# Optimization experiments

Hardware: AMD Instinct MI355X
Metric: run time of the kernel (lower is better)

Reference implementation:

```python
import jax, jax.numpy as jnp
import numpy as np

TAU_MIN, TAU_MAX = 1.5, 4.0
NUM_EXPERTS, TOP_K = 8, 2
V_TH = 1.0
BN_EPS = 1e-5
SG_ALPHA = 4.0  # spikingjelly Sigmoid surrogate default

@jax.custom_vjp
def spike(v):
    # Heaviside spike with sigmoid surrogate gradient
    return (v >= 0.0).astype(v.dtype)

def _spike_fwd(v):
    return spike(v), v

def _spike_bwd(v, g):
    s = jax.nn.sigmoid(SG_ALPHA * v)
    return (g * SG_ALPHA * s * (1.0 - s),)

spike.defvjp(_spike_fwd, _spike_bwd)

def lif(x, tau):
    # MultiStepLIFNode, v_reset=0 (hard reset), detach_reset=True. x: (T, ...)
    def step(v, xt):
        v = v + (xt - v) / tau          # charge
        s = spike(v - V_TH)             # fire
        v = v * (1.0 - jax.lax.stop_gradient(s))  # detached hard reset
        return v, s
    return jax.lax.scan(step, jnp.zeros_like(x[0]), x)[1]

def conv1x1(x, W, b):
    # x: (T,B,Cin,H,W), W: (Cout,Cin) -> (T,B,Cout,H,W)
    return jnp.einsum('tbchw,oc->tbohw', x, W) + b[None, None, :, None, None]

def bn_eval(x, scale, bias):
    # eval-mode BatchNorm2d with running_mean=0, running_var=1
    inv = scale / jnp.sqrt(1.0 + BN_EPS)
    return x * inv[None, None, :, None, None] + bias[None, None, :, None, None]

def expert_fwd(x, tau, W1, b1, s1, bb1, W2, b2, s2, bb2):
    # MS_MLP_Expert: LIF -> conv1x1 -> BN -> (+res) -> LIF -> conv1x1 -> BN -> (+res)
    identity = x
    h = lif(x, tau)
    h = bn_eval(conv1x1(h, W1, b1), s1, bb1)
    h = identity + h            # res: in_features == hidden_features
    identity = h
    o = lif(h, tau)
    o = bn_eval(conv1x1(o, W2, b2), s2, bb2)
    return o + identity

def moe_forward(x, router_W, router_b, router_bn_scale, router_bn_bias,
                W1, b1, bn1_scale, bn1_bias, W2, b2, bn2_scale, bn2_bias):
    T, B, C, H, W = x.shape
    taus = jnp.linspace(TAU_MIN, TAU_MAX, NUM_EXPERTS).astype(x.dtype)
    # --- SpikeRouter ---
    r = lif(x, 2.0)
    r = bn_eval(conv1x1(r, router_W, router_b), router_bn_scale, router_bn_bias)  # (T,B,E,H,W)
    logits_tb = r.mean(axis=(-2, -1))          # (T,B,E)
    # batch-level temporal routing: aggregate logits over T
    logits = logits_tb.mean(axis=0)            # (B,E)
    probs = jax.nn.softmax(logits, axis=-1)
    topw, topi = jax.lax.top_k(probs, TOP_K)   # (B,k)
    topw = topw / topw.sum(axis=-1, keepdims=True)
    dense_w = jnp.zeros((B, NUM_EXPERTS), dtype=x.dtype).at[
        jnp.arange(B)[:, None], topi].set(topw)  # (B,E)
    # --- experts: each processes the full temporal sequence ---
    ys = jax.vmap(expert_fwd, in_axes=(None, 0, 0, 0, 0, 0, 0, 0, 0, 0))(
        x, taus, W1, b1, bn1_scale, bn1_bias, W2, b2, bn2_scale, bn2_bias)  # (E,T,B,C,H,W)
    out = jnp.einsum('etbchw,be->tbchw', ys, dense_w)
    return out

def setup_inputs() -> dict:
    key = jax.random.key(0)
    ks = jax.random.split(key, 6)
    T, B, C, H, Wd = 4, 16, 384, 16, 16
    E = NUM_EXPERTS
    wscale = 1.0 / np.sqrt(C)
    return {
        'x': jax.random.normal(ks[0], (T, B, C, H, Wd), jnp.float32),
        'router_W': jax.random.normal(ks[1], (E, C), jnp.float32) * wscale,
        'router_b': jnp.zeros((E,), jnp.float32),
        'router_bn_scale': jnp.ones((E,), jnp.float32),
        'router_bn_bias': jnp.zeros((E,), jnp.float32),
        'W1': jax.random.normal(ks[2], (E, C, C), jnp.float32) * wscale,
        'b1': jnp.zeros((E, C), jnp.float32),
        'bn1_scale': jnp.ones((E, C), jnp.float32),
        'bn1_bias': jnp.zeros((E, C), jnp.float32),
        'W2': jax.random.normal(ks[3], (E, C, C), jnp.float32) * wscale,
        'b2': jnp.zeros((E, C), jnp.float32),
        'bn2_scale': jnp.ones((E, C), jnp.float32),
        'bn2_bias': jnp.zeros((E, C), jnp.float32),
    }

def reference(x, router_W, router_b, router_bn_scale, router_bn_bias,
              W1, b1, bn1_scale, bn1_bias, W2, b2, bn2_scale, bn2_bias):
    return moe_forward(x, router_W, router_b, router_bn_scale, router_bn_bias,
                       W1, b1, bn1_scale, bn1_bias, W2, b2, bn2_scale, bn2_bias)
```

## Files before the change

### kernel.cpp

```cpp
#include <hip/hip_runtime.h>
#include <math.h>

#define T_  4
#define B_  16
#define C_  384
#define HW_ 256
#define E_  8

typedef __attribute__((ext_vector_type(8))) __bf16 bf16x8;
typedef __attribute__((ext_vector_type(4))) float f32x4;

union FragU { uint4 u; bf16x8 v; };

__device__ __forceinline__ float tau_of(int e) {
    if (e == 7) return 4.0f;
    const float delta = 2.5f / 7.0f;
    return __fadd_rn(1.5f, __fmul_rn((float)e, delta));
}

__device__ __forceinline__ FragU expand_mask(unsigned m) {
    FragU f;
    f.u.x = ((m & 1u)   ? 0x3F80u : 0u) | ((m & 2u)   ? 0x3F800000u : 0u);
    f.u.y = ((m & 4u)   ? 0x3F80u : 0u) | ((m & 8u)   ? 0x3F800000u : 0u);
    f.u.z = ((m & 16u)  ? 0x3F80u : 0u) | ((m & 32u)  ? 0x3F800000u : 0u);
    f.u.w = ((m & 64u)  ? 0x3F80u : 0u) | ((m & 128u) ? 0x3F800000u : 0u);
    return f;
}

__global__ __launch_bounds__(256) void k_prep(const float* __restrict__ x,
        const float* __restrict__ W1, const float* __restrict__ W2,
        unsigned short* __restrict__ Whif, unsigned short* __restrict__ Wlof,
        float* __restrict__ m) {
    if (blockIdx.x < 1152) {
        int tid = blockIdx.x * 256 + threadIdx.x;
        int l = tid & 63;
        int f = tid >> 6;
        int osub = f % 24;
        int ksub = (f / 24) % 12;
        int cv = (f / 288) & 1;
        int e = f / 576;
        const float* Wsrc = (cv == 0 ? W1 : W2) + (size_t)e * C_ * C_;
        int o = osub * 16 + (l & 15);
        int c0 = ksub * 32 + (l >> 4) * 8;
        const float* src = Wsrc + (size_t)o * C_ + c0;
        unsigned hw[8], lw[8];
#pragma unroll
        for (int j = 0; j < 8; ++j) {
            float w = src[j];
            unsigned u = __float_as_uint(w);
            unsigned hi = (u + 0x7FFFu + ((u >> 16) & 1u)) >> 16;
            float hf = __uint_as_float(hi << 16);
            float res = __fsub_rn(w, hf);
            unsigned ru = __float_as_uint(res);
            unsigned lo = (ru + 0x7FFFu + ((ru >> 16) & 1u)) >> 16;
            hw[j] = hi & 0xFFFFu;
            lw[j] = lo & 0xFFFFu;
        }
        size_t dst = (size_t)f * 512 + (size_t)l * 8;
        uint4 hv = make_uint4(hw[0] | (hw[1] << 16), hw[2] | (hw[3] << 16),
                              hw[4] | (hw[5] << 16), hw[6] | (hw[7] << 16));
        uint4 lv = make_uint4(lw[0] | (lw[1] << 16), lw[2] | (lw[3] << 16),
                              lw[4] | (lw[5] << 16), lw[6] | (lw[7] << 16));
        *reinterpret_cast<uint4*>(Whif + dst) = hv;
        *reinterpret_cast<uint4*>(Wlof + dst) = lv;
    } else {
        int bc = blockIdx.x - 1152;
        int b = bc / C_, c = bc % C_;
        int p = threadIdx.x;
        int wv = threadIdx.x >> 6;
        __shared__ int cnt[T_][4];
        float v = 0.0f;
#pragma unroll
        for (int t = 0; t < T_; ++t) {
            float xv = x[((t * B_ + b) * C_ + c) * HW_ + p];
            v = __fadd_rn(v, __fdiv_rn(__fsub_rn(xv, v), 2.0f));
            bool s = (__fsub_rn(v, 1.0f) >= 0.0f);
            if (s) v = 0.0f;
            unsigned long long mask = __ballot(s);
            if ((threadIdx.x & 63) == 0) cnt[t][wv] = (int)__popcll(mask);
        }
        __syncthreads();
        if (threadIdx.x < T_) {
            int t = threadIdx.x;
            int tot = cnt[t][0] + cnt[t][1] + cnt[t][2] + cnt[t][3];
            m[(t * B_ + b) * C_ + c] = (float)tot * 0.00390625f;
        }
    }
}

__device__ __forceinline__ void conv_mfma2(const unsigned short* __restrict__ Whif,
                                           const unsigned short* __restrict__ Wlof,
                                           unsigned base,
                                           const unsigned char* __restrict__ sf,
                                           f32x4 (&acc)[3][4],
                                           int wv, int lane) {
    const unsigned lane8 = (unsigned)lane * 8u;
    const unsigned wbase = base + (unsigned)(wv * 3) * 512u + lane8;
    const unsigned char* fp = sf + lane * 16;
    FragU c0f, c1f, c2f, n0f, n1f, n2f, bf[T_];
    c0f.u = *reinterpret_cast<const uint4*>(Wlof + wbase);
    c1f.u = *reinterpret_cast<const uint4*>(Wlof + wbase + 512u);
    c2f.u = *reinterpret_cast<const uint4*>(Wlof + wbase + 1024u);
#pragma unroll 1
    for (int ksub = 0; ksub < 12; ++ksub) {
        unsigned fo = wbase + (unsigned)ksub * 24u * 512u;
        const unsigned char* fk = fp + ksub * 4096;
#pragma unroll
        for (int t = 0; t < T_; ++t)
            bf[t].u = *reinterpret_cast<const uint4*>(fk + t * 1024);
        n0f.u = *reinterpret_cast<const uint4*>(Whif + fo);
        n1f.u = *reinterpret_cast<const uint4*>(Whif + fo + 512u);
        n2f.u = *reinterpret_cast<const uint4*>(Whif + fo + 1024u);
#pragma unroll
        for (int t = 0; t < T_; ++t) {
            acc[0][t] = __builtin_amdgcn_mfma_f32_16x16x32_bf16(c0f.v, bf[t].v, acc[0][t], 0, 0, 0);
            acc[1][t] = __builtin_amdgcn_mfma_f32_16x16x32_bf16(c1f.v, bf[t].v, acc[1][t], 0, 0, 0);
            acc[2][t] = __builtin_amdgcn_mfma_f32_16x16x32_bf16(c2f.v, bf[t].v, acc[2][t], 0, 0, 0);
        }
        if (ksub < 11) {
            unsigned fn = fo + 24u * 512u;
            c0f.u = *reinterpret_cast<const uint4*>(Wlof + fn);
            c1f.u = *reinterpret_cast<const uint4*>(Wlof + fn + 512u);
            c2f.u = *reinterpret_cast<const uint4*>(Wlof + fn + 1024u);
        }
#pragma unroll
        for (int t = 0; t < T_; ++t) {
            acc[0][t] = __builtin_amdgcn_mfma_f32_16x16x32_bf16(n0f.v, bf[t].v, acc[0][t], 0, 0, 0);
            acc[1][t] = __builtin_amdgcn_mfma_f32_16x16x32_bf16(n1f.v, bf[t].v, acc[1][t], 0, 0, 0);
            acc[2][t] = __builtin_amdgcn_mfma_f32_16x16x32_bf16(n2f.v, bf[t].v, acc[2][t], 0, 0, 0);
        }
    }
}

__global__ __launch_bounds__(1024, 1) void k_expert(
        const float* __restrict__ x, const float* __restrict__ m,
        const float* __restrict__ rW, const float* __restrict__ rb,
        const float* __restrict__ rbs, const float* __restrict__ rbb,
        const unsigned short* __restrict__ Whif, const unsigned short* __restrict__ Wlof,
        const float* __restrict__ b1, const float* __restrict__ s1sc, const float* __restrict__ s1bi,
        const float* __restrict__ b2, const float* __restrict__ s2sc, const float* __restrict__ s2bi,
        float* __restrict__ out) {
    int blk = blockIdx.x;
    int b = (blk & 7) | (((blk >> 3) & 1) << 3);
    int ptile = blk >> 4;

    __shared__ __align__(16) unsigned char sfrag[2][49152];
    __shared__ float bns[2 * 7 * C_];
    __shared__ float lg[E_];
    __shared__ float wsl[2];
    __shared__ int esl[2];

    int tid = threadIdx.x;
    int wave = tid >> 6;
    int rank = wave >> 3;
    int wv = wave & 7;
    int rtid = tid & 511;
    int lane = tid & 63;
    int q = lane >> 4;
    int pl = lane & 15;
    int p = ptile * 16 + pl;
    float denom = sqrtf(__fadd_rn(1.0f, 1e-5f));

    if (tid < 64) {
        int combo = tid & 31, half = tid >> 5;
        int e = combo >> 2, t = combo & 3;
        float dot = 0.0f;
        int c0 = half * 192;
        for (int c = 0; c < 192; ++c)
            dot = fmaf(rW[e * C_ + c0 + c], m[(t * B_ + b) * C_ + c0 + c], dot);
        dot += __shfl_down(dot, 32);
        float Ar = __fdiv_rn(rbs[e], denom);
        float lt = __fadd_rn(__fmul_rn(__fadd_rn(dot, rb[e]), Ar), rbb[e]);
        lt = __fadd_rn(lt, __shfl_xor(lt, 1));
        lt = __fadd_rn(lt, __shfl_xor(lt, 2));
        if (half == 0 && t == 0) lg[e] = __fmul_rn(lt, 0.25f);
    }
    __syncthreads();
    if (tid == 0) {
        float pr[E_];
        float mx = lg[0];
        for (int i = 1; i < E_; ++i) mx = fmaxf(mx, lg[i]);
        float s = 0.0f;
        for (int i = 0; i < E_; ++i) { pr[i] = expf(__fsub_rn(lg[i], mx)); s = __fadd_rn(s, pr[i]); }
        for (int i = 0; i < E_; ++i) pr[i] = __fdiv_rn(pr[i], s);
        int i0 = 0;
        for (int i = 1; i < E_; ++i) if (pr[i] > pr[i0]) i0 = i;
        int i1 = (i0 == 0) ? 1 : 0;
        for (int i = 0; i < E_; ++i) if (i != i0 && pr[i] > pr[i1]) i1 = i;
        float s2 = __fadd_rn(pr[i0], pr[i1]);
        wsl[0] = __fdiv_rn(pr[i0], s2);
        wsl[1] = __fdiv_rn(pr[i1], s2);
        esl[0] = i0;
        esl[1] = i1;
    }
    __syncthreads();

    int er = esl[rank];
    float wr = wsl[rank];
    float taur = tau_of(er);

    if (rtid < C_) {
        float* bp = bns + rank * 7 * C_;
        float a1 = __fdiv_rn(s1sc[er * C_ + rtid], denom);
        float a2 = __fdiv_rn(s2sc[er * C_ + rtid], denom);
        bp[0 * C_ + rtid] = a1;
        bp[1 * C_ + rtid] = b1[er * C_ + rtid];
        bp[2 * C_ + rtid] = s1bi[er * C_ + rtid];
        bp[3 * C_ + rtid] = a2;
        bp[4 * C_ + rtid] = b2[er * C_ + rtid];
        bp[5 * C_ + rtid] = s2bi[er * C_ + rtid];
        bp[6 * C_ + rtid] = __fdiv_rn(1.0f, a2);
    }

    unsigned char* sf = &sfrag[rank][0];
#pragma unroll 1
    for (int task = rtid; task < 48 * 16; task += 512) {
        int cb = task >> 4;
        int tpl = task & 15;
        int tp = ptile * 16 + tpl;
        unsigned char* dst = sf + (cb >> 2) * 4096 + (((cb & 3) * 16 + tpl) * 16);
        float v[8];
#pragma unroll
        for (int j = 0; j < 8; ++j) v[j] = 0.0f;
#pragma unroll
        for (int t = 0; t < T_; ++t) {
            int gbase = ((t * B_ + b) * C_ + cb * 8) * HW_ + tp;
            unsigned d0 = 0, d1 = 0, d2 = 0, d3 = 0;
#pragma unroll
            for (int j = 0; j < 8; ++j) {
                float xv = x[gbase + j * HW_];
                v[j] = __fadd_rn(v[j], __fdiv_rn(__fsub_rn(xv, v[j]), taur));
                bool s = (__fsub_rn(v[j], 1.0f) >= 0.0f);
                if (s) v[j] = 0.0f;
                unsigned bitv = s ? ((j & 1) ? 0x3F800000u : 0x3F80u) : 0u;
                if (j < 2) d0 |= bitv;
                else if (j < 4) d1 |= bitv;
                else if (j < 6) d2 |= bitv;
                else d3 |= bitv;
            }
            *reinterpret_cast<uint4*>(dst + t * 1024) = make_uint4(d0, d1, d2, d3);
        }
    }
    __syncthreads();

    f32x4 acc[3][T_];
#pragma unroll
    for (int os = 0; os < 3; ++os)
#pragma unroll
        for (int t = 0; t < T_; ++t) acc[os][t] = (f32x4)0.0f;
    unsigned base1 = (unsigned)(er * 2) * 12u * 24u * 512u;
    conv_mfma2(Whif, Wlof, base1, sf, acc, wv, lane);

    const float* bp = bns + rank * 7 * C_;
    unsigned pk[3];
#pragma unroll
    for (int os = 0; os < 3; ++os) {
        float v2s[4] = {0.f, 0.f, 0.f, 0.f};
        unsigned pkos = 0;
#pragma unroll
        for (int t = 0; t < T_; ++t) {
            unsigned nb = 0;
#pragma unroll
            for (int r = 0; r < 4; ++r) {
                int o = wv * 48 + os * 16 + q * 4 + r;
                int gi = ((t * B_ + b) * C_ + o) * HW_ + p;
                float y = acc[os][t][r];
                float h = __fadd_rn(x[gi],
                    __fadd_rn(__fmul_rn(__fadd_rn(y, bp[1 * C_ + o]), bp[0 * C_ + o]),
                              bp[2 * C_ + o]));
                v2s[r] = __fadd_rn(v2s[r], __fdiv_rn(__fsub_rn(h, v2s[r]), taur));
                if (__fsub_rn(v2s[r], 1.0f) >= 0.0f) { nb |= (1u << r); v2s[r] = 0.f; }
                acc[os][t][r] = __fmul_rn(h, bp[6 * C_ + o]);
            }
            unsigned nb_hi = (unsigned)__shfl_down((int)nb, 16);
            pkos |= ((nb | (nb_hi << 4)) & 0xFFu) << (8 * t);
        }
        pk[os] = pkos;
    }
    __syncthreads();

    if ((q & 1) == 0) {
#pragma unroll
        for (int os = 0; os < 3; ++os) {
            int g = wv * 6 + os * 2 + (q >> 1);
            unsigned char* dst = sf + (g >> 2) * 4096 + (((g & 3) * 16 + pl) * 16);
#pragma unroll
            for (int t = 0; t < T_; ++t) {
                FragU f = expand_mask((pk[os] >> (8 * t)) & 0xFFu);
                *reinterpret_cast<uint4*>(dst + t * 1024) = f.u;
            }
        }
    }
    __syncthreads();

    unsigned base2 = (unsigned)(er * 2 + 1) * 12u * 24u * 512u;
    conv_mfma2(Whif, Wlof, base2, sf, acc, wv, lane);

    __syncthreads();

    float* pcomb = reinterpret_cast<float*>(&sfrag[0][0]);
    if (rank == 0) {
#pragma unroll
        for (int os = 0; os < 3; ++os)
#pragma unroll
            for (int t = 0; t < T_; ++t)
#pragma unroll
                for (int r = 0; r < 4; ++r) {
                    int o = wv * 48 + os * 16 + q * 4 + r;
                    float y = acc[os][t][r];
                    float val = __fadd_rn(__fmul_rn(__fadd_rn(y, bp[4 * C_ + o]),
                                                    bp[3 * C_ + o]),
                                          bp[5 * C_ + o]);
                    pcomb[(t * C_ + o) * 16 + pl] = __fmul_rn(wr, val);
                }
    }
    __syncthreads();
    if (rank == 1) {
#pragma unroll
        for (int os = 0; os < 3; ++os)
#pragma unroll
            for (int t = 0; t < T_; ++t)
#pragma unroll
                for (int r = 0; r < 4; ++r) {
                    int o = wv * 48 + os * 16 + q * 4 + r;
                    int gi = ((t * B_ + b) * C_ + o) * HW_ + p;
                    float y = acc[os][t][r];
                    float val = __fadd_rn(__fmul_rn(__fadd_rn(y, bp[4 * C_ + o]),
                                                    bp[3 * C_ + o]),
                                          bp[5 * C_ + o]);
                    out[gi] = __fadd_rn(pcomb[(t * C_ + o) * 16 + pl],
                                        __fmul_rn(wr, val));
                }
    }
}

extern "C" void kernel_launch(void* const* d_in, const int* in_sizes, int n_in,
                              void* d_out, int out_size, void* d_ws, size_t ws_size,
                              hipStream_t stream) {
    const float* x    = (const float*)d_in[0];
    const float* rW   = (const float*)d_in[1];
    const float* rb   = (const float*)d_in[2];
    const float* rbs  = (const float*)d_in[3];
    const float* rbb  = (const float*)d_in[4];
    const float* W1   = (const float*)d_in[5];
    const float* b1   = (const float*)d_in[6];
    const float* s1sc = (const float*)d_in[7];
    const float* s1bi = (const float*)d_in[8];
    const float* W2   = (const float*)d_in[9];
    const float* b2   = (const float*)d_in[10];
    const float* s2sc = (const float*)d_in[11];
    const float* s2bi = (const float*)d_in[12];
    float* out = (float*)d_out;

    unsigned short* Whif = (unsigned short*)d_ws;
    unsigned short* Wlof = Whif + 2359296;
    float* m = (float*)((char*)d_ws + 9437184);

    hipLaunchKernelGGL(k_prep, dim3(1152 + B_ * C_), dim3(256), 0, stream,
                       x, W1, W2, Whif, Wlof, m);
    hipLaunchKernelGGL(k_expert, dim3(256), dim3(1024), 0, stream,
                       x, m, rW, rb, rbs, rbb, Whif, Wlof,
                       b1, s1sc, s1bi, b2, s2sc, s2bi, out);
}
```

Baseline: 186.3 us.

## Split expert ranks into separate blocks and combine outputs via atomicAdd

```diff
diff --git a/kernel.cpp b/kernel.cpp
--- a/kernel.cpp
+++ b/kernel.cpp
@@ -132,7 +132,7 @@
     }
 }
 
-__global__ __launch_bounds__(1024, 1) void k_expert(
+__global__ __launch_bounds__(512, 4) void k_expert(
         const float* __restrict__ x, const float* __restrict__ m,
         const float* __restrict__ rW, const float* __restrict__ rb,
         const float* __restrict__ rbs, const float* __restrict__ rbb,
@@ -141,20 +141,18 @@
         const float* __restrict__ b2, const float* __restrict__ s2sc, const float* __restrict__ s2bi,
         float* __restrict__ out) {
     int blk = blockIdx.x;
-    int b = (blk & 7) | (((blk >> 3) & 1) << 3);
-    int ptile = blk >> 4;
-
-    __shared__ __align__(16) unsigned char sfrag[2][49152];
-    __shared__ float bns[2 * 7 * C_];
+    int rank = blk & 1;
+    int b = (blk >> 1) & 15;
+    int ptile = blk >> 5;
+
+    __shared__ __align__(16) unsigned char sfrag[49152];
+    __shared__ float bns[7 * C_];
     __shared__ float lg[E_];
     __shared__ float wsl[2];
     __shared__ int esl[2];
 
     int tid = threadIdx.x;
-    int wave = tid >> 6;
-    int rank = wave >> 3;
-    int wv = wave & 7;
-    int rtid = tid & 511;
+    int wv = tid >> 6;
     int lane = tid & 63;
     int q = lane >> 4;
     int pl = lane & 15;
@@ -199,26 +197,24 @@
     float wr = wsl[rank];
     float taur = tau_of(er);
 
-    if (rtid < C_) {
-        float* bp = bns + rank * 7 * C_;
-        float a1 = __fdiv_rn(s1sc[er * C_ + rtid], denom);
-        float a2 = __fdiv_rn(s2sc[er * C_ + rtid], denom);
-        bp[0 * C_ + rtid] = a1;
-        bp[1 * C_ + rtid] = b1[er * C_ + rtid];
-        bp[2 * C_ + rtid] = s1bi[er * C_ + rtid];
-        bp[3 * C_ + rtid] = a2;
-        bp[4 * C_ + rtid] = b2[er * C_ + rtid];
-        bp[5 * C_ + rtid] = s2bi[er * C_ + rtid];
-        bp[6 * C_ + rtid] = __fdiv_rn(1.0f, a2);
-    }
-
-    unsigned char* sf = &sfrag[rank][0];
+    if (tid < C_) {
+        float a1 = __fdiv_rn(s1sc[er * C_ + tid], denom);
+        float a2 = __fdiv_rn(s2sc[er * C_ + tid], denom);
+        bns[0 * C_ + tid] = a1;
+        bns[1 * C_ + tid] = b1[er * C_ + tid];
+        bns[2 * C_ + tid] = s1bi[er * C_ + tid];
+        bns[3 * C_ + tid] = a2;
+        bns[4 * C_ + tid] = b2[er * C_ + tid];
+        bns[5 * C_ + tid] = s2bi[er * C_ + tid];
+        bns[6 * C_ + tid] = __fdiv_rn(1.0f, a2);
+    }
+
 #pragma unroll 1
-    for (int task = rtid; task < 48 * 16; task += 512) {
+    for (int task = tid; task < 48 * 16; task += 512) {
         int cb = task >> 4;
         int tpl = task & 15;
         int tp = ptile * 16 + tpl;
-        unsigned char* dst = sf + (cb >> 2) * 4096 + (((cb & 3) * 16 + tpl) * 16);
+        unsigned char* dst = sfrag + (cb >> 2) * 4096 + (((cb & 3) * 16 + tpl) * 16);
         float v[8];
 #pragma unroll
         for (int j = 0; j < 8; ++j) v[j] = 0.0f;
@@ -249,9 +245,8 @@
 #pragma unroll
         for (int t = 0; t < T_; ++t) acc[os][t] = (f32x4)0.0f;
     unsigned base1 = (unsigned)(er * 2) * 12u * 24u * 512u;
-    conv_mfma2(Whif, Wlof, base1, sf, acc, wv, lane);
-
-    const float* bp = bns + rank * 7 * C_;
+    conv_mfma2(Whif, Wlof, base1, sfrag, acc, wv, lane);
+
     unsigned pk[3];
 #pragma unroll
     for (int os = 0; os < 3; ++os) {
@@ -266,11 +261,11 @@
                 int gi = ((t * B_ + b) * C_ + o) * HW_ + p;
                 float y = acc[os][t][r];
                 float h = __fadd_rn(x[gi],
-                    __fadd_rn(__fmul_rn(__fadd_rn(y, bp[1 * C_ + o]), bp[0 * C_ + o]),
-                              bp[2 * C_ + o]));
+                    __fadd_rn(__fmul_rn(__fadd_rn(y, bns[1 * C_ + o]), bns[0 * C_ + o]),
+                              bns[2 * C_ + o]));
                 v2s[r] = __fadd_rn(v2s[r], __fdiv_rn(__fsub_rn(h, v2s[r]), taur));
                 if (__fsub_rn(v2s[r], 1.0f) >= 0.0f) { nb |= (1u << r); v2s[r] = 0.f; }
-                acc[os][t][r] = __fmul_rn(h, bp[6 * C_ + o]);
+                acc[os][t][r] = __fmul_rn(h, bns[6 * C_ + o]);
             }
             unsigned nb_hi = (unsigned)__shfl_down((int)nb, 16);
             pkos |= ((nb | (nb_hi << 4)) & 0xFFu) << (8 * t);
@@ -283,7 +278,7 @@
 #pragma unroll
         for (int os = 0; os < 3; ++os) {
             int g = wv * 6 + os * 2 + (q >> 1);
-            unsigned char* dst = sf + (g >> 2) * 4096 + (((g & 3) * 16 + pl) * 16);
+            unsigned char* dst = sfrag + (g >> 2) * 4096 + (((g & 3) * 16 + pl) * 16);
 #pragma unroll
             for (int t = 0; t < T_; ++t) {
                 FragU f = expand_mask((pk[os] >> (8 * t)) & 0xFFu);
@@ -294,44 +289,22 @@
     __syncthreads();
 
     unsigned base2 = (unsigned)(er * 2 + 1) * 12u * 24u * 512u;
-    conv_mfma2(Whif, Wlof, base2, sf, acc, wv, lane);
-
-    __syncthreads();
-
-    float* pcomb = reinterpret_cast<float*>(&sfrag[0][0]);
-    if (rank == 0) {
-#pragma unroll
-        for (int os = 0; os < 3; ++os)
-#pragma unroll
-            for (int t = 0; t < T_; ++t)
-#pragma unroll
-                for (int r = 0; r < 4; ++r) {
-                    int o = wv * 48 + os * 16 + q * 4 + r;
-                    float y = acc[os][t][r];
-                    float val = __fadd_rn(__fmul_rn(__fadd_rn(y, bp[4 * C_ + o]),
-                                                    bp[3 * C_ + o]),
-                                          bp[5 * C_ + o]);
-                    pcomb[(t * C_ + o) * 16 + pl] = __fmul_rn(wr, val);
-                }
-    }
-    __syncthreads();
-    if (rank == 1) {
-#pragma unroll
-        for (int os = 0; os < 3; ++os)
-#pragma unroll
-            for (int t = 0; t < T_; ++t)
-#pragma unroll
-                for (int r = 0; r < 4; ++r) {
-                    int o = wv * 48 + os * 16 + q * 4 + r;
-                    int gi = ((t * B_ + b) * C_ + o) * HW_ + p;
-                    float y = acc[os][t][r];
-                    float val = __fadd_rn(__fmul_rn(__fadd_rn(y, bp[4 * C_ + o]),
-                                                    bp[3 * C_ + o]),
-                                          bp[5 * C_ + o]);
-                    out[gi] = __fadd_rn(pcomb[(t * C_ + o) * 16 + pl],
-                                        __fmul_rn(wr, val));
-                }
-    }
+    conv_mfma2(Whif, Wlof, base2, sfrag, acc, wv, lane);
+
+#pragma unroll
+    for (int os = 0; os < 3; ++os)
+#pragma unroll
+        for (int t = 0; t < T_; ++t)
+#pragma unroll
+            for (int r = 0; r < 4; ++r) {
+                int o = wv * 48 + os * 16 + q * 4 + r;
+                int gi = ((t * B_ + b) * C_ + o) * HW_ + p;
+                float y = acc[os][t][r];
+                float val = __fadd_rn(__fmul_rn(__fadd_rn(y, bns[4 * C_ + o]),
+                                                bns[3 * C_ + o]),
+                                      bns[5 * C_ + o]);
+                atomicAdd(out + gi, __fmul_rn(wr, val));
+            }
 }
 
 extern "C" void kernel_launch(void* const* d_in, const int* in_sizes, int n_in,
@@ -358,7 +331,8 @@
 
     hipLaunchKernelGGL(k_prep, dim3(1152 + B_ * C_), dim3(256), 0, stream,
                        x, W1, W2, Whif, Wlof, m);
-    hipLaunchKernelGGL(k_expert, dim3(256), dim3(1024), 0, stream,
+    hipMemsetAsync(d_out, 0, out_size, stream);
+    hipLaunchKernelGGL(k_expert, dim3(512), dim3(512), 0, stream,
                        x, m, rW, rb, rbs, rbb, Whif, Wlof,
                        b1, s1sc, s1bi, b2, s2sc, s2bi, out);
 }
```

Measured after the change: 215.2 us. +15.5%, slower.

## Process both experts sequentially in 512-thread blocks; stage weight split through LDS

Applied to the files above, without the earlier changes.

```diff
diff --git a/kernel.cpp b/kernel.cpp
--- a/kernel.cpp
+++ b/kernel.cpp
@@ -31,40 +31,49 @@
         const float* __restrict__ W1, const float* __restrict__ W2,
         unsigned short* __restrict__ Whif, unsigned short* __restrict__ Wlof,
         float* __restrict__ m) {
-    if (blockIdx.x < 1152) {
-        int tid = blockIdx.x * 256 + threadIdx.x;
-        int l = tid & 63;
-        int f = tid >> 6;
-        int osub = f % 24;
-        int ksub = (f / 24) % 12;
-        int cv = (f / 288) & 1;
-        int e = f / 576;
-        const float* Wsrc = (cv == 0 ? W1 : W2) + (size_t)e * C_ * C_;
-        int o = osub * 16 + (l & 15);
-        int c0 = ksub * 32 + (l >> 4) * 8;
-        const float* src = Wsrc + (size_t)o * C_ + c0;
-        unsigned hw[8], lw[8];
-#pragma unroll
-        for (int j = 0; j < 8; ++j) {
-            float w = src[j];
-            unsigned u = __float_as_uint(w);
-            unsigned hi = (u + 0x7FFFu + ((u >> 16) & 1u)) >> 16;
-            float hf = __uint_as_float(hi << 16);
-            float res = __fsub_rn(w, hf);
-            unsigned ru = __float_as_uint(res);
-            unsigned lo = (ru + 0x7FFFu + ((ru >> 16) & 1u)) >> 16;
-            hw[j] = hi & 0xFFFFu;
-            lw[j] = lo & 0xFFFFu;
-        }
-        size_t dst = (size_t)f * 512 + (size_t)l * 8;
-        uint4 hv = make_uint4(hw[0] | (hw[1] << 16), hw[2] | (hw[3] << 16),
-                              hw[4] | (hw[5] << 16), hw[6] | (hw[7] << 16));
-        uint4 lv = make_uint4(lw[0] | (lw[1] << 16), lw[2] | (lw[3] << 16),
-                              lw[4] | (lw[5] << 16), lw[6] | (lw[7] << 16));
-        *reinterpret_cast<uint4*>(Whif + dst) = hv;
-        *reinterpret_cast<uint4*>(Wlof + dst) = lv;
+    if (blockIdx.x < 384) {
+        int idx = blockIdx.x;
+        int og = idx % 24;
+        int cv = (idx / 24) & 1;
+        int e = idx / 48;
+        const float* Wsrc = (cv == 0 ? W1 : W2) + (size_t)e * C_ * C_
+                            + (size_t)og * 16 * C_;
+        __shared__ float ld[16 * 388];
+        int tid = threadIdx.x;
+        for (int i = tid; i < 16 * 384; i += 256) {
+            int r = i >> 8; r = i / 384;
+            int c = i - r * 384;
+            ld[r * 388 + c] = Wsrc[i];
+        }
+        __syncthreads();
+        unsigned fbase = ((unsigned)(e * 2 + cv) * 12u * 24u + (unsigned)og) * 512u;
+        for (int s = tid; s < 768; s += 256) {
+            int l = s & 63;
+            int ksub = s >> 6;
+            const float* src = ld + (l & 15) * 388 + ksub * 32 + (l >> 4) * 8;
+            unsigned hw[8], lw[8];
+#pragma unroll
+            for (int j = 0; j < 8; ++j) {
+                float w = src[j];
+                unsigned u = __float_as_uint(w);
+                unsigned hi = (u + 0x7FFFu + ((u >> 16) & 1u)) >> 16;
+                float hf = __uint_as_float(hi << 16);
+                float res = __fsub_rn(w, hf);
+                unsigned ru = __float_as_uint(res);
+                unsigned lo = (ru + 0x7FFFu + ((ru >> 16) & 1u)) >> 16;
+                hw[j] = hi & 0xFFFFu;
+                lw[j] = lo & 0xFFFFu;
+            }
+            size_t dst = (size_t)fbase + (size_t)ksub * 24u * 512u + (size_t)l * 8;
+            uint4 hv = make_uint4(hw[0] | (hw[1] << 16), hw[2] | (hw[3] << 16),
+                                  hw[4] | (hw[5] << 16), hw[6] | (hw[7] << 16));
+            uint4 lv = make_uint4(lw[0] | (lw[1] << 16), lw[2] | (lw[3] << 16),
+                                  lw[4] | (lw[5] << 16), lw[6] | (lw[7] << 16));
+            *reinterpret_cast<uint4*>(Whif + dst) = hv;
+            *reinterpret_cast<uint4*>(Wlof + dst) = lv;
+        }
     } else {
-        int bc = blockIdx.x - 1152;
+        int bc = blockIdx.x - 384;
         int b = bc / C_, c = bc % C_;
         int p = threadIdx.x;
         int wv = threadIdx.x >> 6;
@@ -132,7 +141,7 @@
     }
 }
 
-__global__ __launch_bounds__(1024, 1) void k_expert(
+__global__ __launch_bounds__(512, 2) void k_expert(
         const float* __restrict__ x, const float* __restrict__ m,
         const float* __restrict__ rW, const float* __restrict__ rb,
         const float* __restrict__ rbs, const float* __restrict__ rbb,
@@ -144,17 +153,16 @@
     int b = (blk & 7) | (((blk >> 3) & 1) << 3);
     int ptile = blk >> 4;
 
-    __shared__ __align__(16) unsigned char sfrag[2][49152];
+    __shared__ __align__(16) unsigned char sfrag[49152];
+    __shared__ unsigned char s1m1[3072];
+    __shared__ unsigned char s2mb[3072];
     __shared__ float bns[2 * 7 * C_];
     __shared__ float lg[E_];
     __shared__ float wsl[2];
     __shared__ int esl[2];
 
     int tid = threadIdx.x;
-    int wave = tid >> 6;
-    int rank = wave >> 3;
-    int wv = wave & 7;
-    int rtid = tid & 511;
+    int wv = tid >> 6;
     int lane = tid & 63;
     int q = lane >> 4;
     int pl = lane & 15;
@@ -195,127 +203,111 @@
     }
     __syncthreads();
 
-    int er = esl[rank];
-    float wr = wsl[rank];
-    float taur = tau_of(er);
-
-    if (rtid < C_) {
-        float* bp = bns + rank * 7 * C_;
-        float a1 = __fdiv_rn(s1sc[er * C_ + rtid], denom);
-        float a2 = __fdiv_rn(s2sc[er * C_ + rtid], denom);
-        bp[0 * C_ + rtid] = a1;
-        bp[1 * C_ + rtid] = b1[er * C_ + rtid];
-        bp[2 * C_ + rtid] = s1bi[er * C_ + rtid];
-        bp[3 * C_ + rtid] = a2;
-        bp[4 * C_ + rtid] = b2[er * C_ + rtid];
-        bp[5 * C_ + rtid] = s2bi[er * C_ + rtid];
-        bp[6 * C_ + rtid] = __fdiv_rn(1.0f, a2);
-    }
-
-    unsigned char* sf = &sfrag[rank][0];
+    int e0 = esl[0], e1 = esl[1];
+    float wr0 = wsl[0], wr1 = wsl[1];
+    float tau0 = tau_of(e0), tau1 = tau_of(e1);
+
+    if (tid < C_) {
+#pragma unroll
+        for (int r_ = 0; r_ < 2; ++r_) {
+            int er = (r_ == 0) ? e0 : e1;
+            float* bp = bns + r_ * 7 * C_;
+            float a1 = __fdiv_rn(s1sc[er * C_ + tid], denom);
+            float a2 = __fdiv_rn(s2sc[er * C_ + tid], denom);
+            bp[0 * C_ + tid] = a1;
+            bp[1 * C_ + tid] = b1[er * C_ + tid];
+            bp[2 * C_ + tid] = s1bi[er * C_ + tid];
+            bp[3 * C_ + tid] = a2;
+            bp[4 * C_ + tid] = b2[er * C_ + tid];
+            bp[5 * C_ + tid] = s2bi[er * C_ + tid];
+            bp[6 * C_ + tid] = __fdiv_rn(1.0f, a2);
+        }
+    }
+
 #pragma unroll 1
-    for (int task = rtid; task < 48 * 16; task += 512) {
+    for (int task = tid; task < 48 * 16; task += 512) {
         int cb = task >> 4;
         int tpl = task & 15;
         int tp = ptile * 16 + tpl;
-        unsigned char* dst = sf + (cb >> 2) * 4096 + (((cb & 3) * 16 + tpl) * 16);
-        float v[8];
-#pragma unroll
-        for (int j = 0; j < 8; ++j) v[j] = 0.0f;
+        unsigned char* dst0 = sfrag + (cb >> 2) * 4096 + (((cb & 3) * 16 + tpl) * 16);
+        float va[8], vb[8];
+#pragma unroll
+        for (int j = 0; j < 8; ++j) { va[j] = 0.0f; vb[j] = 0.0f; }
 #pragma unroll
         for (int t = 0; t < T_; ++t) {
             int gbase = ((t * B_ + b) * C_ + cb * 8) * HW_ + tp;
-            unsigned d0 = 0, d1 = 0, d2 = 0, d3 = 0;
+            unsigned d0 = 0, d1 = 0, d2 = 0, d3 = 0, mb1 = 0;
 #pragma unroll
             for (int j = 0; j < 8; ++j) {
                 float xv = x[gbase + j * HW_];
-                v[j] = __fadd_rn(v[j], __fdiv_rn(__fsub_rn(xv, v[j]), taur));
-                bool s = (__fsub_rn(v[j], 1.0f) >= 0.0f);
-                if (s) v[j] = 0.0f;
-                unsigned bitv = s ? ((j & 1) ? 0x3F800000u : 0x3F80u) : 0u;
+                va[j] = __fadd_rn(va[j], __fdiv_rn(__fsub_rn(xv, va[j]), tau0));
+                bool s0 = (__fsub_rn(va[j], 1.0f) >= 0.0f);
+                if (s0) va[j] = 0.0f;
+                unsigned bitv = s0 ? ((j & 1) ? 0x3F800000u : 0x3F80u) : 0u;
                 if (j < 2) d0 |= bitv;
                 else if (j < 4) d1 |= bitv;
                 else if (j < 6) d2 |= bitv;
                 else d3 |= bitv;
+                vb[j] = __fadd_rn(vb[j], __fdiv_rn(__fsub_rn(xv, vb[j]), tau1));
+                bool s1 = (__fsub_rn(vb[j], 1.0f) >= 0.0f);
+                if (s1) { mb1 |= (1u << j); vb[j] = 0.0f; }
             }
-            *reinterpret_cast<uint4*>(dst + t * 1024) = make_uint4(d0, d1, d2, d3);
+            *reinterpret_cast<uint4*>(dst0 + t * 1024) = make_uint4(d0, d1, d2, d3);
+            s1m1[(t * 16 + tpl) * 48 + cb] = (unsigned char)mb1;
         }
     }
     __syncthreads();
 
     f32x4 acc[3][T_];
+
 #pragma unroll
     for (int os = 0; os < 3; ++os)
 #pragma unroll
         for (int t = 0; t < T_; ++t) acc[os][t] = (f32x4)0.0f;
-    unsigned base1 = (unsigned)(er * 2) * 12u * 24u * 512u;
-    conv_mfma2(Whif, Wlof, base1, sf, acc, wv, lane);
-
-    const float* bp = bns + rank * 7 * C_;
-    unsigned pk[3];
-#pragma unroll
-    for (int os = 0; os < 3; ++os) {
-        float v2s[4] = {0.f, 0.f, 0.f, 0.f};
-        unsigned pkos = 0;
-#pragma unroll
-        for (int t = 0; t < T_; ++t) {
-            unsigned nb = 0;
-#pragma unroll
-            for (int r = 0; r < 4; ++r) {
-                int o = wv * 48 + os * 16 + q * 4 + r;
-                int gi = ((t * B_ + b) * C_ + o) * HW_ + p;
-                float y = acc[os][t][r];
-                float h = __fadd_rn(x[gi],
-                    __fadd_rn(__fmul_rn(__fadd_rn(y, bp[1 * C_ + o]), bp[0 * C_ + o]),
-                              bp[2 * C_ + o]));
-                v2s[r] = __fadd_rn(v2s[r], __fdiv_rn(__fsub_rn(h, v2s[r]), taur));
-                if (__fsub_rn(v2s[r], 1.0f) >= 0.0f) { nb |= (1u << r); v2s[r] = 0.f; }
-                acc[os][t][r] = __fmul_rn(h, bp[6 * C_ + o]);
-            }
-            unsigned nb_hi = (unsigned)__shfl_down((int)nb, 16);
-            pkos |= ((nb | (nb_hi << 4)) & 0xFFu) << (8 * t);
-        }
-        pk[os] = pkos;
-    }
-    __syncthreads();
-
-    if ((q & 1) == 0) {
+    conv_mfma2(Whif, Wlof, (unsigned)(e0 * 2) * 12u * 24u * 512u, sfrag, acc, wv, lane);
+
+    {
+        const float* bp = bns;
 #pragma unroll
         for (int os = 0; os < 3; ++os) {
-            int g = wv * 6 + os * 2 + (q >> 1);
-            unsigned char* dst = sf + (g >> 2) * 4096 + (((g & 3) * 16 + pl) * 16);
+            float v2s[4] = {0.f, 0.f, 0.f, 0.f};
 #pragma unroll
             for (int t = 0; t < T_; ++t) {
-                FragU f = expand_mask((pk[os] >> (8 * t)) & 0xFFu);
-                *reinterpret_cast<uint4*>(dst + t * 1024) = f.u;
-            }
-        }
-    }
-    __syncthreads();
-
-    unsigned base2 = (unsigned)(er * 2 + 1) * 12u * 24u * 512u;
-    conv_mfma2(Whif, Wlof, base2, sf, acc, wv, lane);
-
-    __syncthreads();
-
-    float* pcomb = reinterpret_cast<float*>(&sfrag[0][0]);
-    if (rank == 0) {
-#pragma unroll
-        for (int os = 0; os < 3; ++os)
-#pragma unroll
-            for (int t = 0; t < T_; ++t)
+                unsigned nb = 0;
 #pragma unroll
                 for (int r = 0; r < 4; ++r) {
                     int o = wv * 48 + os * 16 + q * 4 + r;
+                    int gi = ((t * B_ + b) * C_ + o) * HW_ + p;
                     float y = acc[os][t][r];
-                    float val = __fadd_rn(__fmul_rn(__fadd_rn(y, bp[4 * C_ + o]),
-                                                    bp[3 * C_ + o]),
-                                          bp[5 * C_ + o]);
-                    pcomb[(t * C_ + o) * 16 + pl] = __fmul_rn(wr, val);
+                    float h = __fadd_rn(x[gi],
+                        __fadd_rn(__fmul_rn(__fadd_rn(y, bp[1 * C_ + o]), bp[0 * C_ + o]),
+                                  bp[2 * C_ + o]));
+                    v2s[r] = __fadd_rn(v2s[r], __fdiv_rn(__fsub_rn(h, v2s[r]), tau0));
+                    if (__fsub_rn(v2s[r], 1.0f) >= 0.0f) { nb |= (1u << r); v2s[r] = 0.f; }
+                    acc[os][t][r] = __fmul_rn(h, bp[6 * C_ + o]);
                 }
-    }
-    __syncthreads();
-    if (rank == 1) {
+                unsigned nb_hi = (unsigned)__shfl_down((int)nb, 16);
+                if ((q & 1) == 0)
+                    s2mb[(t * 16 + pl) * 48 + (wv * 6 + os * 2 + (q >> 1))] =
+                        (unsigned char)(nb | (nb_hi << 4));
+            }
+        }
+    }
+    __syncthreads();
+
+#pragma unroll
+    for (int it = 0; it < 6; ++it) {
+        int s = tid + it * 512;
+        int l = s & 63, t = (s >> 6) & 3, ks = s >> 8;
+        FragU f = expand_mask(s2mb[(t * 16 + (l & 15)) * 48 + ks * 4 + (l >> 4)]);
+        *reinterpret_cast<uint4*>(sfrag + ks * 4096 + t * 1024 + l * 16) = f.u;
+    }
+    __syncthreads();
+
+    conv_mfma2(Whif, Wlof, (unsigned)(e0 * 2 + 1) * 12u * 24u * 512u, sfrag, acc, wv, lane);
+
+    {
+        const float* bp = bns;
 #pragma unroll
         for (int os = 0; os < 3; ++os)
 #pragma unroll
@@ -328,8 +320,81 @@
                     float val = __fadd_rn(__fmul_rn(__fadd_rn(y, bp[4 * C_ + o]),
                                                     bp[3 * C_ + o]),
                                           bp[5 * C_ + o]);
-                    out[gi] = __fadd_rn(pcomb[(t * C_ + o) * 16 + pl],
-                                        __fmul_rn(wr, val));
+                    out[gi] = __fmul_rn(wr0, val);
+                }
+    }
+    __syncthreads();
+
+#pragma unroll
+    for (int it = 0; it < 6; ++it) {
+        int s = tid + it * 512;
+        int l = s & 63, t = (s >> 6) & 3, ks = s >> 8;
+        FragU f = expand_mask(s1m1[(t * 16 + (l & 15)) * 48 + ks * 4 + (l >> 4)]);
+        *reinterpret_cast<uint4*>(sfrag + ks * 4096 + t * 1024 + l * 16) = f.u;
+    }
+    __syncthreads();
+
+#pragma unroll
+    for (int os = 0; os < 3; ++os)
+#pragma unroll
+        for (int t = 0; t < T_; ++t) acc[os][t] = (f32x4)0.0f;
+    conv_mfma2(Whif, Wlof, (unsigned)(e1 * 2) * 12u * 24u * 512u, sfrag, acc, wv, lane);
+
+    {
+        const float* bp = bns + 7 * C_;
+#pragma unroll
+        for (int os = 0; os < 3; ++os) {
+            float v2s[4] = {0.f, 0.f, 0.f, 0.f};
+#pragma unroll
+            for (int t = 0; t < T_; ++t) {
+                unsigned nb = 0;
+#pragma unroll
+                for (int r = 0; r < 4; ++r) {
+                    int o = wv * 48 + os * 16 + q * 4 + r;
+                    int gi = ((t * B_ + b) * C_ + o) * HW_ + p;
+                    float y = acc[os][t][r];
+                    float h = __fadd_rn(x[gi],
+                        __fadd_rn(__fmul_rn(__fadd_rn(y, bp[1 * C_ + o]), bp[0 * C_ + o]),
+                                  bp[2 * C_ + o]));
+                    v2s[r] = __fadd_rn(v2s[r], __fdiv_rn(__fsub_rn(h, v2s[r]), tau1));
+                    if (__fsub_rn(v2s[r], 1.0f) >= 0.0f) { nb |= (1u << r); v2s[r] = 0.f; }
+                    acc[os][t][r] = __fmul_rn(h, bp[6 * C_ + o]);
+                }
+                unsigned nb_hi = (unsigned)__shfl_down((int)nb, 16);
+                if ((q & 1) == 0)
+                    s2mb[(t * 16 + pl) * 48 + (wv * 6 + os * 2 + (q >> 1))] =
+                        (unsigned char)(nb | (nb_hi << 4));
+            }
+        }
+    }
+    __syncthreads();
+
+#pragma unroll
+    for (int it = 0; it < 6; ++it) {
+        int s = tid + it * 512;
+        int l = s & 63, t = (s >> 6) & 3, ks = s >> 8;
+        FragU f = expand_mask(s2mb[(t * 16 + (l & 15)) * 48 + ks * 4 + (l >> 4)]);
+        *reinterpret_cast<uint4*>(sfrag + ks * 4096 + t * 1024 + l * 16) = f.u;
+    }
+    __syncthreads();
+
+    conv_mfma2(Whif, Wlof, (unsigned)(e1 * 2 + 1) * 12u * 24u * 512u, sfrag, acc, wv, lane);
+
+    {
+        const float* bp = bns + 7 * C_;
+#pragma unroll
+        for (int os = 0; os < 3; ++os)
+#pragma unroll
+            for (int t = 0; t < T_; ++t)
+#pragma unroll
+                for (int r = 0; r < 4; ++r) {
+                    int o = wv * 48 + os * 16 + q * 4 + r;
+                    int gi = ((t * B_ + b) * C_ + o) * HW_ + p;
+                    float y = acc[os][t][r];
+                    float val = __fadd_rn(__fmul_rn(__fadd_rn(y, bp[4 * C_ + o]),
+                                                    bp[3 * C_ + o]),
+                                          bp[5 * C_ + o]);
+                    out[gi] = __fadd_rn(out[gi], __fmul_rn(wr1, val));
                 }
     }
 }
@@ -356,9 +421,9 @@
     unsigned short* Wlof = Whif + 2359296;
     float* m = (float*)((char*)d_ws + 9437184);
 
-    hipLaunchKernelGGL(k_prep, dim3(1152 + B_ * C_), dim3(256), 0, stream,
+    hipLaunchKernelGGL(k_prep, dim3(384 + B_ * C_), dim3(256), 0, stream,
                        x, W1, W2, Whif, Wlof, m);
-    hipLaunchKernelGGL(k_expert, dim3(256), dim3(1024), 0, stream,
+    hipLaunchKernelGGL(k_expert, dim3(256), dim3(512), 0, stream,
                        x, m, rW, rb, rbs, rbb, Whif, Wlof,
                        b1, s1sc, s1bi, b2, s2sc, s2bi, out);
 }
```

Result: no change. 189.1 us (+1.5%).
